# Kernel tuning notes

Measured on AMD Instinct MI355X. Metric: run time of the kernel, lower is better.

## Reference

```python
import jax, jax.numpy as jnp
import numpy as np

DIM = 1024
NUM_HEADS = 16
DIM_PROJ = int(2 / 3 * 4 * DIM // 8 * 8)  # 2728, per source
EPS = 1e-5


def rms_norm(x, g):
    # NOTE: source computes sqrt(mean(x^2)) then divides by (rms + eps)
    rms = jnp.sqrt(jnp.mean(x * x, axis=-1, keepdims=True))
    return x / (rms + EPS) * g


def alibi_slopes(num_heads):
    base = (2.0 ** 8) ** (1.0 / num_heads)
    return jnp.asarray([1.0 / base ** (i + 1) for i in range(num_heads)], dtype=jnp.float32)


def setup_inputs() -> dict:
    key = jax.random.key(0)
    ks = jax.random.split(key, 7)
    B, T, C, P = 2, 2048, DIM, DIM_PROJ
    s = 0.02
    return {
        "x": jax.random.normal(ks[0], (B, T, C), dtype=jnp.float32),
        "g1": jnp.ones((C,), dtype=jnp.float32),
        "w_qkv": jax.random.normal(ks[1], (C, 3 * C), dtype=jnp.float32) * s,
        "w_o": jax.random.normal(ks[2], (C, C), dtype=jnp.float32) * s,
        "g2": jnp.ones((C,), dtype=jnp.float32),
        "W": jax.random.normal(ks[3], (C, P), dtype=jnp.float32) * s,
        "V": jax.random.normal(ks[4], (C, P), dtype=jnp.float32) * s,
        "W2": jax.random.normal(ks[5], (P, C), dtype=jnp.float32) * s,
    }


def reference(x, g1, w_qkv, w_o, g2, W, V, W2):
    B, T, C = x.shape
    H = NUM_HEADS
    Dh = C // H

    # --- attention sublayer ---
    h = rms_norm(x, g1)
    qkv = h @ w_qkv                              # [B,T,3C]
    q, k, v = jnp.split(qkv, 3, axis=-1)
    q = q.reshape(B, T, H, Dh).transpose(0, 2, 1, 3)  # [B,H,T,Dh]
    k = k.reshape(B, T, H, Dh).transpose(0, 2, 1, 3)
    v = v.reshape(B, T, H, Dh).transpose(0, 2, 1, 3)

    wei = jnp.einsum('bhqd,bhkd->bhqk', q, k)
    pos = jnp.arange(T)
    rel = (pos[None, :] - pos[:, None]).astype(jnp.float32)  # [T,T]
    m = alibi_slopes(H)[:, None, None]                        # [H,1,1]
    scale = C ** 0.5                                          # sqrt(dim), per source
    scores = wei / scale + m * rel
    causal = pos[None, :] <= pos[:, None]                     # [T,T]
    scores = jnp.where(causal[None, None], scores, -jnp.inf)
    attn = jax.nn.softmax(scores, axis=-1)

    out = jnp.einsum('bhqk,bhkd->bhqd', attn, v)
    concat = out.transpose(0, 2, 1, 3).reshape(B, T, C)
    x = concat @ w_o + x

    # --- SwiGLU sublayer ---
    h = rms_norm(x, g2)
    gated = jax.nn.silu(h @ W) * (h @ V)
    return gated @ W2 + x
```

## Files before the change

### kernel.cpp

```cpp
#include <hip/hip_runtime.h>
#include <math.h>

typedef __attribute__((ext_vector_type(8))) short bf16x8;
typedef __attribute__((ext_vector_type(4))) float f32x4;
typedef __attribute__((ext_vector_type(16))) float f32x16;

static __device__ __forceinline__ short f2bf(float x){
  union { float f; unsigned u; } a; a.f = x;
  unsigned r = a.u + 0x7fffu + ((a.u >> 16) & 1u);
  return (short)(r >> 16);
}

static __device__ __forceinline__ unsigned cvtpk(float lo, float hi){
  unsigned r; asm("v_cvt_pk_bf16_f32 %0, %1, %2" : "=v"(r) : "v"(lo), "v"(hi)); return r;
}

__global__ __launch_bounds__(256) void transpose_bf16_kernel(
    const float* __restrict__ in, short* __restrict__ out,
    int IR, int IC, int OR, int OC)
{
  __shared__ float tile[32][33];
  int i0 = blockIdx.x * 32;
  int j0 = blockIdx.y * 32;
  int tx = threadIdx.x, ty = threadIdx.y;
  #pragma unroll
  for (int r = 0; r < 32; r += 8){
    int j = j0 + ty + r, i = i0 + tx;
    tile[ty + r][tx] = (j < IR && i < IC) ? in[(size_t)j * IC + i] : 0.f;
  }
  __syncthreads();
  #pragma unroll
  for (int r = 0; r < 32; r += 8){
    int oi = i0 + ty + r, oj = j0 + tx;
    if (oi < OR && oj < OC) out[(size_t)oi * OC + oj] = f2bf(tile[tx][ty + r]);
  }
}

__global__ __launch_bounds__(256) void transpose_bb_kernel(
    const short* __restrict__ in, short* __restrict__ out)
{
  __shared__ short tile[32][33];
  int bh = blockIdx.z;
  int t0 = blockIdx.x * 32;
  int d0 = blockIdx.y * 32;
  int tx = threadIdx.x, ty = threadIdx.y;
  const short* src = in + ((size_t)bh * 2048 + t0) * 64 + d0;
  #pragma unroll
  for (int r = 0; r < 32; r += 8)
    tile[ty + r][tx] = src[(size_t)(ty + r) * 64 + tx];
  __syncthreads();
  short* dst = out + ((size_t)bh * 64 + d0) * 2048 + t0;
  #pragma unroll
  for (int r = 0; r < 32; r += 8)
    dst[(size_t)(ty + r) * 2048 + tx] = tile[tx][ty + r];
}

__global__ __launch_bounds__(256) void rmsnorm_kernel(
    const float* __restrict__ x, const float* __restrict__ g, short* __restrict__ out)
{
  int row = blockIdx.x, tid = threadIdx.x;
  const float4* xr = (const float4*)(x + (size_t)row * 1024);
  float4 v = xr[tid];
  float ss = v.x*v.x + v.y*v.y + v.z*v.z + v.w*v.w;
  #pragma unroll
  for (int m = 1; m < 64; m <<= 1) ss += __shfl_xor(ss, m, 64);
  __shared__ float sm[4];
  if ((tid & 63) == 0) sm[tid >> 6] = ss;
  __syncthreads();
  float tot = sm[0] + sm[1] + sm[2] + sm[3];
  float inv = 1.f / (sqrtf(tot * (1.f/1024.f)) + 1e-5f);
  float4 gv = ((const float4*)g)[tid];
  short4 o;
  o.x = f2bf(v.x * inv * gv.x);
  o.y = f2bf(v.y * inv * gv.y);
  o.z = f2bf(v.z * inv * gv.z);
  o.w = f2bf(v.w * inv * gv.w);
  *(short4*)(out + (size_t)row * 1024 + tid * 4) = o;
}

enum { EPI_F32 = 0, EPI_RESID = 1, EPI_QKV = 2 };

template<int BM, int BN>
static __device__ __forceinline__ void dp_issue(
    const short* __restrict__ A, const short* __restrict__ Bt,
    short* __restrict__ lbuf, int K, int m0, int n0, int k0,
    int wave, int lane, int l)
{
  int g = (l * 8 + wave) * 64 + lane;
  const short* src;
  if (g < BM * 8){
    int row = g >> 3, cc = g & 7;
    src = A + (size_t)(m0 + row) * K + k0 + ((cc ^ (row & 7)) << 3);
  } else {
    int gb = g - BM * 8;
    int row = gb >> 3, cc = gb & 7;
    src = Bt + (size_t)(n0 + row) * K + k0 + ((cc ^ (row & 7)) << 3);
  }
  __builtin_amdgcn_global_load_lds((const __attribute__((address_space(1))) void*)src,
                                   (__attribute__((address_space(3))) void*)(lbuf + (size_t)g * 8),
                                   16, 0, 0);
}

template<int BM, int BN, int EPI>
__global__ __launch_bounds__(512, 2) void gemm_dp_kernel(
    const short* __restrict__ A, const short* __restrict__ Bt,
    int M, int N, int K,
    float* __restrict__ outF, short* __restrict__ outB,
    const float* __restrict__ resid,
    short* __restrict__ qb, short* __restrict__ kb, short* __restrict__ vb)
{
  constexpr int L  = (BM + BN) / 64;
  constexpr int WM = BM / 2, WN = BN / 4;
  constexpr int FR = WM / 16, FC = WN / 16;
  __shared__ short lds[2][(BM + BN) * 64];
  const int tid = threadIdx.x, lane = tid & 63, wave = tid >> 6;
  const int wr = wave >> 2, wc = wave & 3;
  const int la = lane & 15, lg = lane >> 4;

  int nbn = N / BN;
  int nwg = (M / BM) * nbn;
  int bid = blockIdx.x;
  int wg = ((nwg & 7) == 0) ? ((bid & 7) * (nwg >> 3) + (bid >> 3)) : bid;
  int m0 = (wg / nbn) * BM, n0 = (wg % nbn) * BN;

  f32x4 acc[FR][FC];
  #pragma unroll
  for (int i = 0; i < FR; ++i)
    #pragma unroll
    for (int j = 0; j < FC; ++j) acc[i][j] = f32x4{0.f, 0.f, 0.f, 0.f};

  const int NT = K >> 6;

  #pragma unroll
  for (int l = 0; l < L; ++l) dp_issue<BM, BN>(A, Bt, lds[0], K, m0, n0, 0,  wave, lane, l);
  #pragma unroll
  for (int l = 0; l < L; ++l) dp_issue<BM, BN>(A, Bt, lds[1], K, m0, n0, 64, wave, lane, l);

  for (int t = 0; t < NT; ++t){
    short* curb = lds[t & 1];
    if (t + 1 < NT){
      if constexpr (L == 8)      asm volatile("s_waitcnt vmcnt(8)" ::: "memory");
      else if constexpr (L == 6) asm volatile("s_waitcnt vmcnt(6)" ::: "memory");
      else                       asm volatile("s_waitcnt vmcnt(4)" ::: "memory");
    } else {
      asm volatile("s_waitcnt vmcnt(0)" ::: "memory");
    }
    __builtin_amdgcn_s_barrier();
    __builtin_amdgcn_sched_barrier(0);

    #pragma unroll
    for (int qr = 0; qr < FR / 4; ++qr){
      #pragma unroll
      for (int qc = 0; qc < FC / 2; ++qc){
        bf16x8 af[4][2], bfv[2][2];
        #pragma unroll
        for (int ii = 0; ii < 4; ++ii){
          int r = wr * WM + (qr * 4 + ii) * 16 + la;
          #pragma unroll
          for (int ks = 0; ks < 2; ++ks)
            af[ii][ks] = *(const bf16x8*)(curb + r * 64 + (((ks * 4 + lg) ^ (r & 7)) << 3));
        }
        #pragma unroll
        for (int jc = 0; jc < 2; ++jc){
          int rb = wc * WN + (qc * 2 + jc) * 16 + la;
          #pragma unroll
          for (int ks = 0; ks < 2; ++ks)
            bfv[jc][ks] = *(const bf16x8*)(curb + BM * 64 + rb * 64 + (((ks * 4 + lg) ^ (rb & 7)) << 3));
        }
        __builtin_amdgcn_s_setprio(1);
        #pragma unroll
        for (int ii = 0; ii < 4; ++ii)
          #pragma unroll
          for (int jc = 0; jc < 2; ++jc){
            acc[qr*4+ii][qc*2+jc] = __builtin_amdgcn_mfma_f32_16x16x32_bf16(
                af[ii][0], bfv[jc][0], acc[qr*4+ii][qc*2+jc], 0, 0, 0);
            acc[qr*4+ii][qc*2+jc] = __builtin_amdgcn_mfma_f32_16x16x32_bf16(
                af[ii][1], bfv[jc][1], acc[qr*4+ii][qc*2+jc], 0, 0, 0);
          }
        __builtin_amdgcn_s_setprio(0);
      }
    }
    __builtin_amdgcn_sched_barrier(0);
    __builtin_amdgcn_s_barrier();
    __builtin_amdgcn_sched_barrier(0);
    if (t + 2 < NT){
      #pragma unroll
      for (int l = 0; l < L; ++l)
        dp_issue<BM, BN>(A, Bt, curb, K, m0, n0, (t + 2) << 6, wave, lane, l);
    }
  }

  #pragma unroll
  for (int i = 0; i < FR; ++i){
    #pragma unroll
    for (int j = 0; j < FC; ++j){
      #pragma unroll
      for (int rr = 0; rr < 4; ++rr){
        int row = m0 + wr * WM + i * 16 + lg * 4 + rr;
        int col = n0 + wc * WN + j * 16 + la;
        float v = acc[i][j][rr];
        size_t idx = (size_t)row * N + col;
        if (EPI == EPI_F32){
          outF[idx] = v;
        } else if (EPI == EPI_RESID){
          outF[idx] = v + resid[idx];
        } else {
          int which = col >> 10;
          int hh = (col & 1023) >> 6;
          int d = col & 63;
          int bb = row >> 11, tt = row & 2047;
          size_t o = (((size_t)(bb * 16 + hh) * 2048) + tt) * 64 + d;
          if (which == 0)      qb[o] = f2bf(v * 0.045084220f);
          else if (which == 1) kb[o] = f2bf(v);
          else                 vb[o] = f2bf(v);
        }
      }
    }
  }
}

static __device__ __forceinline__ void wv_issue(
    const short* __restrict__ A, const short* __restrict__ Bw, const short* __restrict__ Bv,
    short* __restrict__ lbuf, int K, int m0, int n0, int k0,
    int wave, int lane, int l)
{
  int g = (l * 8 + wave) * 64 + lane;
  const short* src;
  if (g < 1024){
    int row = g >> 3, cc = g & 7;
    src = A + (size_t)(m0 + row) * K + k0 + ((cc ^ (row & 7)) << 3);
  } else if (g < 2048){
    int gb = g - 1024;
    int row = gb >> 3, cc = gb & 7;
    src = Bw + (size_t)(n0 + row) * K + k0 + ((cc ^ (row & 7)) << 3);
  } else {
    int gb = g - 2048;
    int row = gb >> 3, cc = gb & 7;
    src = Bv + (size_t)(n0 + row) * K + k0 + ((cc ^ (row & 7)) << 3);
  }
  __builtin_amdgcn_global_load_lds((const __attribute__((address_space(1))) void*)src,
                                   (__attribute__((address_space(3))) void*)(lbuf + (size_t)g * 8),
                                   16, 0, 0);
}

__global__ __launch_bounds__(512, 2) void gemm_wv_kernel(
    const short* __restrict__ A, const short* __restrict__ Bw, const short* __restrict__ Bv,
    int M, int N, int K, short* __restrict__ outGated)
{
  __shared__ short lds[2][384 * 64];
  const int tid = threadIdx.x, lane = tid & 63, wave = tid >> 6;
  const int wr = wave >> 2, wc = wave & 3;
  const int la = lane & 15, lg = lane >> 4;

  int nbn = N >> 7;
  int nwg = (M >> 7) * nbn;
  int bid = blockIdx.x;
  int wg = ((nwg & 7) == 0) ? ((bid & 7) * (nwg >> 3) + (bid >> 3)) : bid;
  int m0 = (wg / nbn) << 7, n0 = (wg % nbn) << 7;

  f32x4 accW[4][2], accV[4][2];
  #pragma unroll
  for (int i = 0; i < 4; ++i)
    #pragma unroll
    for (int j = 0; j < 2; ++j){
      accW[i][j] = f32x4{0.f, 0.f, 0.f, 0.f};
      accV[i][j] = f32x4{0.f, 0.f, 0.f, 0.f};
    }

  const int NT = K >> 6;

  #pragma unroll
  for (int l = 0; l < 6; ++l) wv_issue(A, Bw, Bv, lds[0], K, m0, n0, 0,  wave, lane, l);
  #pragma unroll
  for (int l = 0; l < 6; ++l) wv_issue(A, Bw, Bv, lds[1], K, m0, n0, 64, wave, lane, l);

  for (int t = 0; t < NT; ++t){
    short* curb = lds[t & 1];
    if (t + 1 < NT) asm volatile("s_waitcnt vmcnt(6)" ::: "memory");
    else            asm volatile("s_waitcnt vmcnt(0)" ::: "memory");
    __builtin_amdgcn_s_barrier();
    __builtin_amdgcn_sched_barrier(0);

    bf16x8 af[4][2], bw[2][2], bv[2][2];
    #pragma unroll
    for (int ii = 0; ii < 4; ++ii){
      int r = wr * 64 + ii * 16 + la;
      #pragma unroll
      for (int ks = 0; ks < 2; ++ks)
        af[ii][ks] = *(const bf16x8*)(curb + r * 64 + (((ks * 4 + lg) ^ (r & 7)) << 3));
    }
    #pragma unroll
    for (int jc = 0; jc < 2; ++jc){
      int rb = wc * 32 + jc * 16 + la;
      #pragma unroll
      for (int ks = 0; ks < 2; ++ks){
        bw[jc][ks] = *(const bf16x8*)(curb +  8192 + rb * 64 + (((ks * 4 + lg) ^ (rb & 7)) << 3));
        bv[jc][ks] = *(const bf16x8*)(curb + 16384 + rb * 64 + (((ks * 4 + lg) ^ (rb & 7)) << 3));
      }
    }
    __builtin_amdgcn_s_setprio(1);
    #pragma unroll
    for (int ii = 0; ii < 4; ++ii)
      #pragma unroll
      for (int jc = 0; jc < 2; ++jc){
        accW[ii][jc] = __builtin_amdgcn_mfma_f32_16x16x32_bf16(af[ii][0], bw[jc][0], accW[ii][jc], 0, 0, 0);
        accW[ii][jc] = __builtin_amdgcn_mfma_f32_16x16x32_bf16(af[ii][1], bw[jc][1], accW[ii][jc], 0, 0, 0);
        accV[ii][jc] = __builtin_amdgcn_mfma_f32_16x16x32_bf16(af[ii][0], bv[jc][0], accV[ii][jc], 0, 0, 0);
        accV[ii][jc] = __builtin_amdgcn_mfma_f32_16x16x32_bf16(af[ii][1], bv[jc][1], accV[ii][jc], 0, 0, 0);
      }
    __builtin_amdgcn_s_setprio(0);
    __builtin_amdgcn_sched_barrier(0);
    __builtin_amdgcn_s_barrier();
    __builtin_amdgcn_sched_barrier(0);
    if (t + 2 < NT){
      #pragma unroll
      for (int l = 0; l < 6; ++l)
        wv_issue(A, Bw, Bv, curb, K, m0, n0, (t + 2) << 6, wave, lane, l);
    }
  }

  #pragma unroll
  for (int i = 0; i < 4; ++i){
    #pragma unroll
    for (int j = 0; j < 2; ++j){
      #pragma unroll
      for (int rr = 0; rr < 4; ++rr){
        int row = m0 + wr * 64 + i * 16 + lg * 4 + rr;
        int col = n0 + wc * 32 + j * 16 + la;
        float gg = accW[i][j][rr];
        float vv = accV[i][j][rr];
        float s = gg / (1.f + __expf(-gg));
        outGated[(size_t)row * N + col] = f2bf(s * vv);
      }
    }
  }
}

#define CBASE(r) ((float)(((r) & 3) + 8 * ((r) >> 2)))
#define CBI(r)   ((((r) & 3) + 8 * ((r) >> 2)))

#define KVLOAD(KF, VF, T_)                                                      \
  do {                                                                          \
    _Pragma("unroll")                                                           \
    for (int ks = 0; ks < 4; ++ks)                                              \
      KF[ks] = *(const bf16x8*)(Kg + ((size_t)((T_) * 32 + q32)) * 64 + ks * 16 + hi * 8); \
    _Pragma("unroll")                                                           \
    for (int dk = 0; dk < 4; ++dk)                                              \
      VF[dk] = *(const bf16x8*)(Vt + ((size_t)((dk >> 1) * 32 + q32)) * 2048 + (T_) * 32 + (dk & 1) * 16 + hi * 8); \
  } while (0)

#define PROC(CK, CV, T_, DOPF, NK, NV)                                          \
  do {                                                                          \
    f32x16 sS;                                                                  \
    _Pragma("unroll") for (int i = 0; i < 16; ++i) sS[i] = 0.f;                 \
    sS = __builtin_amdgcn_mfma_f32_32x32x16_bf16(CK[0], qf[0], sS, 0, 0, 0);    \
    sS = __builtin_amdgcn_mfma_f32_32x32x16_bf16(CK[1], qf[1], sS, 0, 0, 0);    \
    sS = __builtin_amdgcn_mfma_f32_32x32x16_bf16(CK[2], qf[2], sS, 0, 0, 0);    \
    sS = __builtin_amdgcn_mfma_f32_32x32x16_bf16(CK[3], qf[3], sS, 0, 0, 0);    \
    if (DOPF) KVLOAD(NK, NV, (T_) + 2);                                         \
    float bb2 = slope2 * (float)((T_) * 32 + 4 * hi - qpos);                    \
    float sc[16];                                                               \
    _Pragma("unroll")                                                           \
    for (int r = 0; r < 16; ++r) sc[r] = (sS[r] + bb2) + slope2 * CBASE(r);     \
    if ((T_) == j){                                                             \
      _Pragma("unroll")                                                         \
      for (int r = 0; r < 16; ++r)                                              \
        sc[r] = (CBI(r) + 4 * hi <= q32) ? sc[r] : -1e30f;                      \
    }                                                                           \
    float t8[8], t4[4];                                                         \
    _Pragma("unroll") for (int i = 0; i < 8; ++i) t8[i] = fmaxf(sc[i], sc[i + 8]); \
    _Pragma("unroll") for (int i = 0; i < 4; ++i) t4[i] = fmaxf(t8[i], t8[i + 4]); \
    float mx = fmaxf(fmaxf(t4[0], t4[1]), fmaxf(t4[2], t4[3]));                 \
    mx = fmaxf(mx, __shfl_xor(mx, 32, 64));                                     \
    if (!__all(mx <= m_run + 8.f)){                                             \
      float mnew = fmaxf(m_run, mx);                                            \
      float aL = exp2f(m_run - mnew);                                           \
      l_run *= aL;                                                              \
      m_run = mnew;                                                             \
      _Pragma("unroll")                                                         \
      for (int r = 0; r < 16; ++r){                                             \
        float aq = __shfl(aL, CBI(r) + 4 * hi, 64);                             \
        o0[r] *= aq; o1[r] *= aq;                                               \
      }                                                                         \
    }                                                                           \
    float pr[16];                                                               \
    _Pragma("unroll")                                                           \
    for (int r = 0; r < 16; ++r) pr[r] = exp2f(sc[r] - m_run);                  \
    _Pragma("unroll") for (int i = 0; i < 8; ++i) t8[i] = pr[i] + pr[i + 8];    \
    _Pragma("unroll") for (int i = 0; i < 4; ++i) t4[i] = t8[i] + t8[i + 4];    \
    float ps = (t4[0] + t4[1]) + (t4[2] + t4[3]);                               \
    ps += __shfl_xor(ps, 32, 64);                                               \
    l_run += ps;                                                                \
    unsigned c0 = cvtpk(pr[0], pr[1]),   c1 = cvtpk(pr[2], pr[3]);              \
    unsigned c2 = cvtpk(pr[4], pr[5]),   c3 = cvtpk(pr[6], pr[7]);              \
    unsigned c4 = cvtpk(pr[8], pr[9]),   c5 = cvtpk(pr[10], pr[11]);            \
    unsigned c6 = cvtpk(pr[12], pr[13]), c7 = cvtpk(pr[14], pr[15]);            \
    unsigned x0 = (unsigned)__shfl_xor((int)c0, 32, 64), x1 = (unsigned)__shfl_xor((int)c1, 32, 64); \
    unsigned x2 = (unsigned)__shfl_xor((int)c2, 32, 64), x3 = (unsigned)__shfl_xor((int)c3, 32, 64); \
    unsigned x4 = (unsigned)__shfl_xor((int)c4, 32, 64), x5 = (unsigned)__shfl_xor((int)c5, 32, 64); \
    unsigned x6 = (unsigned)__shfl_xor((int)c6, 32, 64), x7 = (unsigned)__shfl_xor((int)c7, 32, 64); \
    union { unsigned u[4]; bf16x8 v; } pa0u, pa1u;                              \
    pa0u.u[0] = hi ? x2 : c0;  pa0u.u[1] = hi ? x3 : c1;                        \
    pa0u.u[2] = hi ? c2 : x0;  pa0u.u[3] = hi ? c3 : x1;                        \
    pa1u.u[0] = hi ? x6 : c4;  pa1u.u[1] = hi ? x7 : c5;                        \
    pa1u.u[2] = hi ? c6 : x4;  pa1u.u[3] = hi ? c7 : x5;                        \
    o0 = __builtin_amdgcn_mfma_f32_32x32x16_bf16(pa0u.v, CV[0], o0, 0, 0, 0);   \
    o0 = __builtin_amdgcn_mfma_f32_32x32x16_bf16(pa1u.v, CV[1], o0, 0, 0, 0);   \
    o1 = __builtin_amdgcn_mfma_f32_32x32x16_bf16(pa0u.v, CV[2], o1, 0, 0, 0);   \
    o1 = __builtin_amdgcn_mfma_f32_32x32x16_bf16(pa1u.v, CV[3], o1, 0, 0, 0);   \
  } while (0)

__global__ __launch_bounds__(512) void attn_kernel(
    const short* __restrict__ qb, const short* __restrict__ kb,
    const short* __restrict__ vtb, short* __restrict__ concat)
{
  const int T = 2048;
  int id = blockIdx.x;
  int grp = id & 7;
  int p   = id >> 3;
  int wid = threadIdx.x >> 6;
  int e   = wid & 3;
  int s   = wid >> 2;
  int bh = grp * 4 + e;
  int lane = threadIdx.x & 63;
  int q32 = lane & 31;
  int hi  = lane >> 5;
  int h = bh & 15, b = bh >> 4;

  __shared__ float partLDS[4][16][64][2];
  __shared__ float mlLDS[4][64][2];

  const short* Q  = qb  + (size_t)bh * T * 64;
  const short* Kg = kb  + (size_t)bh * T * 64;
  const short* Vt = vtb + (size_t)bh * 64 * T;

  float slope2 = exp2f(-0.5f * (float)(h + 1)) * 1.44269504f;

  for (int task = 0; task < 2; ++task){
    int j = task ? (63 - p) : p;
    int q0 = j * 32;
    int qpos = q0 + q32;

    bf16x8 qf[4];
    #pragma unroll
    for (int ks = 0; ks < 4; ++ks)
      qf[ks] = *(const bf16x8*)(Q + (size_t)qpos * 64 + ks * 16 + hi * 8);

    f32x16 o0, o1;
    #pragma unroll
    for (int i = 0; i < 16; ++i){ o0[i] = 0.f; o1[i] = 0.f; }
    float m_run = -1e30f, l_run = 0.f;

    if (s <= j){
      bf16x8 kA[4], vA[4], kB[4], vB[4];
      KVLOAD(kA, vA, s);
      int t = s;
      while (1){
        PROC(kA, vA, t, (t + 2 <= j), kB, vB);
        t += 2; if (t > j) break;
        PROC(kB, vB, t, (t + 2 <= j), kA, vA);
        t += 2; if (t > j) break;
      }
    }

    if (s == 0){
      #pragma unroll
      for (int r2 = 0; r2 < 8; ++r2){
        partLDS[e][r2][lane][0]     = o0[2 * r2];
        partLDS[e][r2][lane][1]     = o0[2 * r2 + 1];
        partLDS[e][r2 + 8][lane][0] = o1[2 * r2];
        partLDS[e][r2 + 8][lane][1] = o1[2 * r2 + 1];
      }
      mlLDS[e][lane][0] = m_run;
      mlLDS[e][lane][1] = l_run;
    }
    __syncthreads();
    if (s == 1){
      float mE = mlLDS[e][lane][0];
      float lE = mlLDS[e][lane][1];
      float mS = fmaxf(mE, m_run);
      float aE = exp2f(mE - mS);
      float aO = exp2f(m_run - mS);
      float lT = aE * lE + aO * l_run;
      float linv = 1.f / lT;
      float fE = aE * linv;
      float fO = aO * linv;
      #pragma unroll
      for (int r = 0; r < 16; ++r){
        int crow = CBI(r) + 4 * hi;
        float fEr = __shfl(fE, crow, 64);
        float fOr = __shfl(fO, crow, 64);
        float oE0 = partLDS[e][r >> 1][lane][r & 1];
        float oE1 = partLDS[e][8 + (r >> 1)][lane][r & 1];
        size_t base = ((size_t)(b * 2048 + q0 + crow)) * 1024 + h * 64;
        concat[base + q32]      = f2bf(fEr * oE0 + fOr * o0[r]);
        concat[base + 32 + q32] = f2bf(fEr * oE1 + fOr * o1[r]);
      }
    }
    __syncthreads();
  }
}

extern "C" void kernel_launch(void* const* d_in, const int* in_sizes, int n_in,
                              void* d_out, int out_size, void* d_ws, size_t ws_size,
                              hipStream_t stream)
{
  (void)in_sizes; (void)n_in; (void)out_size; (void)ws_size;
  const float* x     = (const float*)d_in[0];
  const float* g1    = (const float*)d_in[1];
  const float* w_qkv = (const float*)d_in[2];
  const float* w_o   = (const float*)d_in[3];
  const float* g2    = (const float*)d_in[4];
  const float* W     = (const float*)d_in[5];
  const float* V     = (const float*)d_in[6];
  const float* W2    = (const float*)d_in[7];
  float* out = (float*)d_out;

  char* wsb = (char*)d_ws;
  size_t off = 0;
  auto alloc = [&](size_t bytes) -> void* {
    void* p = wsb + off;
    off += (bytes + 255) & ~(size_t)255;
    return p;
  };
  short* wqkvT = (short*)alloc((size_t)3072 * 1024 * 2);
  short* woT   = (short*)alloc((size_t)1024 * 1024 * 2);
  short* WT    = (short*)alloc((size_t)2816 * 1024 * 2);
  short* VT    = (short*)alloc((size_t)2816 * 1024 * 2);
  short* W2T   = (short*)alloc((size_t)1024 * 2816 * 2);
  short* h1    = (short*)alloc((size_t)4096 * 1024 * 2);
  short* qbuf  = (short*)alloc((size_t)4096 * 1024 * 2);
  short* kbuf  = (short*)alloc((size_t)4096 * 1024 * 2);
  short* vbuf  = (short*)alloc((size_t)4096 * 1024 * 2);
  short* vtbuf = (short*)alloc((size_t)4096 * 1024 * 2);
  short* conc  = (short*)alloc((size_t)4096 * 1024 * 2);
  float* x2    = (float*)alloc((size_t)4096 * 1024 * 4);
  short* h2    = (short*)alloc((size_t)4096 * 1024 * 2);
  short* gated = (short*)alloc((size_t)4096 * 2816 * 2);

  dim3 tb(32, 8);
  hipLaunchKernelGGL(transpose_bf16_kernel, dim3(96, 32), tb, 0, stream, w_qkv, wqkvT, 1024, 3072, 3072, 1024);
  hipLaunchKernelGGL(transpose_bf16_kernel, dim3(32, 32), tb, 0, stream, w_o,   woT,   1024, 1024, 1024, 1024);
  hipLaunchKernelGGL(transpose_bf16_kernel, dim3(88, 32), tb, 0, stream, W,     WT,    1024, 2728, 2816, 1024);
  hipLaunchKernelGGL(transpose_bf16_kernel, dim3(88, 32), tb, 0, stream, V,     VT,    1024, 2728, 2816, 1024);
  hipLaunchKernelGGL(transpose_bf16_kernel, dim3(32, 88), tb, 0, stream, W2,    W2T,   2728, 1024, 1024, 2816);

  hipLaunchKernelGGL(rmsnorm_kernel, dim3(4096), dim3(256), 0, stream, x, g1, h1);

  hipLaunchKernelGGL((gemm_dp_kernel<128, 128, EPI_QKV>), dim3(768), dim3(512), 0, stream,
                     h1, wqkvT, 4096, 3072, 1024,
                     (float*)nullptr, (short*)nullptr, (const float*)nullptr,
                     qbuf, kbuf, vbuf);

  hipLaunchKernelGGL(transpose_bb_kernel, dim3(64, 2, 32), tb, 0, stream, vbuf, vtbuf);

  hipLaunchKernelGGL(attn_kernel, dim3(256), dim3(512), 0, stream, qbuf, kbuf, vtbuf, conc);

  hipLaunchKernelGGL((gemm_dp_kernel<128, 128, EPI_RESID>), dim3(256), dim3(512), 0, stream,
                     conc, woT, 4096, 1024, 1024,
                     x2, (short*)nullptr, x,
                     (short*)nullptr, (short*)nullptr, (short*)nullptr);

  hipLaunchKernelGGL(rmsnorm_kernel, dim3(4096), dim3(256), 0, stream, x2, g2, h2);

  hipLaunchKernelGGL(gemm_wv_kernel, dim3(704), dim3(512), 0, stream,
                     h2, WT, VT, 4096, 2816, 1024, gated);

  hipLaunchKernelGGL((gemm_dp_kernel<128, 128, EPI_RESID>), dim3(256), dim3(512), 0, stream,
                     gated, W2T, 4096, 1024, 2816,
                     out, (short*)nullptr, x2,
                     (short*)nullptr, (short*)nullptr, (short*)nullptr);
}
```

Baseline: 269.2 us.

## Split attention KV range across four waves per head and double the grid

The attention kernel now gives each (batch, head, query tile) four waves that stride over key tiles by four, instead of two waves striding by two, and launches twice as many blocks, each covering two heads. All four partial softmax states are written to shared memory and merged cooperatively, with each wave producing a quarter of the output rows. This is meant to raise parallelism and occupancy for the long causal rows and shorten the per-wave serial chain. In exchange it needs more shared memory per block and does more merge work, with extra exp2 calls and LDS reads.

Result: slower. 279.0 us (+3.6%).

```diff
diff --git a/kernel.cpp b/kernel.cpp
--- a/kernel.cpp
+++ b/kernel.cpp
@@ -336,6 +336,7 @@
   }
 }
 
+
 #define CBASE(r) ((float)(((r) & 3) + 8 * ((r) >> 2)))
 #define CBI(r)   ((((r) & 3) + 8 * ((r) >> 2)))
 
@@ -357,7 +358,7 @@
     sS = __builtin_amdgcn_mfma_f32_32x32x16_bf16(CK[1], qf[1], sS, 0, 0, 0);    \
     sS = __builtin_amdgcn_mfma_f32_32x32x16_bf16(CK[2], qf[2], sS, 0, 0, 0);    \
     sS = __builtin_amdgcn_mfma_f32_32x32x16_bf16(CK[3], qf[3], sS, 0, 0, 0);    \
-    if (DOPF) KVLOAD(NK, NV, (T_) + 2);                                         \
+    if (DOPF) KVLOAD(NK, NV, (T_) + 4);                                         \
     float bb2 = slope2 * (float)((T_) * 32 + 4 * hi - qpos);                    \
     float sc[16];                                                               \
     _Pragma("unroll")                                                           \
@@ -417,18 +418,19 @@
   const int T = 2048;
   int id = blockIdx.x;
   int grp = id & 7;
-  int p   = id >> 3;
+  int sub = (id >> 3) & 1;
+  int p   = id >> 4;
   int wid = threadIdx.x >> 6;
-  int e   = wid & 3;
-  int s   = wid >> 2;
-  int bh = grp * 4 + e;
+  int e   = wid & 1;
+  int s   = wid >> 1;
+  int bh = grp * 4 + sub * 2 + e;
   int lane = threadIdx.x & 63;
   int q32 = lane & 31;
   int hi  = lane >> 5;
   int h = bh & 15, b = bh >> 4;
 
-  __shared__ float partLDS[4][16][64][2];
-  __shared__ float mlLDS[4][64][2];
+  __shared__ float partLDS[2][4][16][64][2];
+  __shared__ float mlLDS[2][4][64][2];
 
   const short* Q  = qb  + (size_t)bh * T * 64;
   const short* Kg = kb  + (size_t)bh * T * 64;
@@ -456,46 +458,53 @@
       KVLOAD(kA, vA, s);
       int t = s;
       while (1){
-        PROC(kA, vA, t, (t + 2 <= j), kB, vB);
-        t += 2; if (t > j) break;
-        PROC(kB, vB, t, (t + 2 <= j), kA, vA);
-        t += 2; if (t > j) break;
-      }
-    }
-
-    if (s == 0){
-      #pragma unroll
-      for (int r2 = 0; r2 < 8; ++r2){
-        partLDS[e][r2][lane][0]     = o0[2 * r2];
-        partLDS[e][r2][lane][1]     = o0[2 * r2 + 1];
-        partLDS[e][r2 + 8][lane][0] = o1[2 * r2];
-        partLDS[e][r2 + 8][lane][1] = o1[2 * r2 + 1];
-      }
-      mlLDS[e][lane][0] = m_run;
-      mlLDS[e][lane][1] = l_run;
-    }
+        PROC(kA, vA, t, (t + 4 <= j), kB, vB);
+        t += 4; if (t > j) break;
+        PROC(kB, vB, t, (t + 4 <= j), kA, vA);
+        t += 4; if (t > j) break;
+      }
+    }
+
+    #pragma unroll
+    for (int r2 = 0; r2 < 8; ++r2){
+      partLDS[e][s][r2][lane][0]     = o0[2 * r2];
+      partLDS[e][s][r2][lane][1]     = o0[2 * r2 + 1];
+      partLDS[e][s][r2 + 8][lane][0] = o1[2 * r2];
+      partLDS[e][s][r2 + 8][lane][1] = o1[2 * r2 + 1];
+    }
+    mlLDS[e][s][lane][0] = m_run;
+    mlLDS[e][s][lane][1] = l_run;
     __syncthreads();
-    if (s == 1){
-      float mE = mlLDS[e][lane][0];
-      float lE = mlLDS[e][lane][1];
-      float mS = fmaxf(mE, m_run);
-      float aE = exp2f(mE - mS);
-      float aO = exp2f(m_run - mS);
-      float lT = aE * lE + aO * l_run;
-      float linv = 1.f / lT;
-      float fE = aE * linv;
-      float fO = aO * linv;
-      #pragma unroll
-      for (int r = 0; r < 16; ++r){
-        int crow = CBI(r) + 4 * hi;
-        float fEr = __shfl(fE, crow, 64);
-        float fOr = __shfl(fO, crow, 64);
-        float oE0 = partLDS[e][r >> 1][lane][r & 1];
-        float oE1 = partLDS[e][8 + (r >> 1)][lane][r & 1];
-        size_t base = ((size_t)(b * 2048 + q0 + crow)) * 1024 + h * 64;
-        concat[base + q32]      = f2bf(fEr * oE0 + fOr * o0[r]);
-        concat[base + 32 + q32] = f2bf(fEr * oE1 + fOr * o1[r]);
-      }
+
+    #pragma unroll
+    for (int k = 0; k < 4; ++k){
+      int r2 = s * 4 + k;
+      int ri = r2 * 2;
+      int rb = ri & 15;
+      int colb = (ri < 16) ? 0 : 32;
+      int crow0 = CBI(rb) + 4 * hi;
+      int crow1 = crow0 + 1;
+
+      float m0v = -1e30f, m1v = -1e30f;
+      #pragma unroll
+      for (int w = 0; w < 4; ++w){
+        m0v = fmaxf(m0v, mlLDS[e][w][crow0][0]);
+        m1v = fmaxf(m1v, mlLDS[e][w][crow1][0]);
+      }
+      float l0v = 0.f, l1v = 0.f, vx = 0.f, vy = 0.f;
+      #pragma unroll
+      for (int w = 0; w < 4; ++w){
+        float a0 = exp2f(mlLDS[e][w][crow0][0] - m0v);
+        float a1 = exp2f(mlLDS[e][w][crow1][0] - m1v);
+        l0v += a0 * mlLDS[e][w][crow0][1];
+        l1v += a1 * mlLDS[e][w][crow1][1];
+        vx  += a0 * partLDS[e][w][r2][lane][0];
+        vy  += a1 * partLDS[e][w][r2][lane][1];
+      }
+      size_t base0 = ((size_t)(b * 2048 + q0 + crow0)) * 1024 + h * 64 + colb + q32;
+      size_t base1 = ((size_t)(b * 2048 + q0 + crow1)) * 1024 + h * 64 + colb + q32;
+      concat[base0] = f2bf(vx / l0v);
+      concat[base1] = f2bf(vy / l1v);
     }
     __syncthreads();
   }
@@ -554,7 +563,7 @@
 
   hipLaunchKernelGGL(transpose_bb_kernel, dim3(64, 2, 32), tb, 0, stream, vbuf, vtbuf);
 
-  hipLaunchKernelGGL(attn_kernel, dim3(256), dim3(512), 0, stream, qbuf, kbuf, vtbuf, conc);
+  hipLaunchKernelGGL(attn_kernel, dim3(512), dim3(512), 0, stream, qbuf, kbuf, vtbuf, conc);
 
   hipLaunchKernelGGL((gemm_dp_kernel<128, 128, EPI_RESID>), dim3(256), dim3(512), 0, stream,
                      conc, woT, 4096, 1024, 1024,
```
